# Kernel optimization log

Measured on AMD Instinct MI355X. Metric: run time of the kernel, lower is better.

## Reference

```python
import jax, jax.numpy as jnp
import numpy as np

B, L, H, S, D = 2, 4096, 16, 64, 128  # batch, seq, num_heads, num_states, head_dim


def setup_inputs() -> dict:
    key = jax.random.key(0)
    k1, k2, k3 = jax.random.split(key, 3)
    return {
        "x": jax.random.normal(k1, (B, L, H, D), dtype=jnp.float32),
        "weight": jax.random.normal(k2, (H, S, D), dtype=jnp.float32),   # nn.Parameter torch.randn
        "bias": jax.random.normal(k3, (H, S), dtype=jnp.float32),
    }


def reference(x, weight, bias):
    b, l, h, d = x.shape
    s = weight.shape[1]
    T = b * l
    # per-head linear router in fp32 (matches x.float()/weight.float() in torch)
    logits = jnp.einsum('blhd,hsd->blhs', x.astype(jnp.float32), weight.astype(jnp.float32)) \
             + bias.astype(jnp.float32)
    score = jax.nn.softmax(logits, axis=-1)                # [B,L,H,S]
    indices = jnp.argmax(score, axis=-1).astype(jnp.int32)  # [B,L,H]
    # GradTop1 forward: all-ones; straight-through backward scatters grad at argmax.
    top = jnp.take_along_axis(score, indices[..., None], axis=-1)[..., 0]
    sg_indices = top - jax.lax.stop_gradient(top) + 1.0      # forward == 1, grad -> one-hot scatter
    # histogram per head over num_states (Triton bincount equivalent)
    flat = indices.reshape(T, h)                             # [T,H]
    counts = jax.vmap(lambda v: jnp.bincount(v, length=s))(flat.T)  # [H,S]
    mean_indices = counts.astype(jnp.float32) / T
    balance_loss = s * jnp.sum(jnp.mean(mean_indices[None, None] * score, axis=(0, 1)))
    return sg_indices.astype(x.dtype), indices, balance_loss.astype(x.dtype)
```

## Files before the change

kernel.cpp:

```cpp
#include <hip/hip_runtime.h>


#define TOKENS  8192
#define NHEAD   16
#define NSTATE  64
#define DDIM    128
#define TH      (TOKENS * NHEAD)

#define WFRAG_BYTES (1u << 19)
#define REP_OFF     WFRAG_BYTES
#define REP_BYTES   65536
#define IDX_OFF     (WFRAG_BYTES + REP_BYTES)

typedef _Float16 half8 __attribute__((ext_vector_type(8)));
typedef float    f32x4 __attribute__((ext_vector_type(4)));

#define GLOAD_LDS16(gsrc, ldst)                                           \
    __builtin_amdgcn_global_load_lds(                                     \
        (const __attribute__((address_space(1))) void*)(gsrc),            \
        (__attribute__((address_space(3))) void*)(ldst), 16, 0, 0)

__device__ __forceinline__ unsigned int ordf(float f) {
    unsigned int u = __float_as_uint(f);
    return (u & 0x80000000u) ? ~u : (u | 0x80000000u);
}

__device__ __forceinline__ void split8(const f32x4 v0, const f32x4 v1,
                                       half8& hh, half8& ll) {
    #pragma unroll
    for (int j = 0; j < 4; ++j) {
        _Float16 h0 = (_Float16)v0[j];
        hh[j]     = h0;  ll[j]     = (_Float16)(v0[j] - (float)h0);
        _Float16 h1 = (_Float16)v1[j];
        hh[4 + j] = h1;  ll[4 + j] = (_Float16)(v1[j] - (float)h1);
    }
}

__global__ __launch_bounds__(256)
void prep_w(const float* __restrict__ w, half8* __restrict__ wfrag,
            float* __restrict__ rep )
{
    const int t    = blockIdx.x * 256 + threadIdx.x;
    rep[t] = 0.0f;
    const int lane = t & 63;
    const int n    = (t >> 6) & 3;
    const int ks   = (t >> 8) & 3;
    const int h    = t >> 10;
    const int s    = n * 16 + (lane & 15);
    const int k0   = ks * 32 + (lane >> 4) * 8;
    const float* src = w + (size_t)(h * NSTATE + s) * DDIM + k0;
    f32x4 v0 = *reinterpret_cast<const f32x4*>(src);
    f32x4 v1 = *reinterpret_cast<const f32x4*>(src + 4);
    half8 hv, lv;
    split8(v0, v1, hv, lv);
    const size_t hb = (size_t)h * 2048;
    const int fb = (ks * 4 + n) * 2;
    wfrag[hb + (size_t)fb * 64 + lane]       = hv;
    wfrag[hb + (size_t)(fb + 1) * 64 + lane] = lv;
}

__global__ __launch_bounds__(256)
void router_mfma(const float* __restrict__ x,
                 const half8* __restrict__ wfrag,
                 const float* __restrict__ bias,
                 float* __restrict__ idx_scr,
                 float* __restrict__ repf,
                 float* __restrict__ repc)
{
    __shared__ __align__(16) unsigned char smem[32768];

    const int blk  = blockIdx.x;
    const int h    = blk & 15;
    const int grp  = blk >> 4;
    const int tid  = threadIdx.x;
    const int wave = __builtin_amdgcn_readfirstlane(tid >> 6);
    const int lane = tid & 63;
    const int col  = lane & 15;
    const int kg   = lane >> 4;
    const int base = grp * 128;

    {
        const char* wsrc = (const char*)wfrag + (size_t)h * 32768;
        #pragma unroll
        for (int i = 0; i < 8; ++i) {
            const int off = (wave * 8 + i) * 1024;
            GLOAD_LDS16(wsrc + off + lane * 16, smem + off);
        }
    }

    const float b0 = bias[h * NSTATE +  0 + col];
    const float b1 = bias[h * NSTATE + 16 + col];
    const float b2 = bias[h * NSTATE + 32 + col];
    const float b3 = bias[h * NSTATE + 48 + col];

    __syncthreads();

    const size_t srow = (size_t)(NHEAD * DDIM);
    float sc[4] = {0.f, 0.f, 0.f, 0.f};
    int   cn[4] = {0, 0, 0, 0};

    #pragma unroll
    for (int tt = 0; tt < 2; ++tt) {
        const int tokb = base + (wave + 4 * tt) * 16;

        const float* arow = x + (size_t)(tokb + col) * srow + h * DDIM + kg * 8;
        f32x4 g[4][2];
        #pragma unroll
        for (int ks = 0; ks < 4; ++ks) {
            g[ks][0] = *reinterpret_cast<const f32x4*>(arow + ks * 32);
            g[ks][1] = *reinterpret_cast<const f32x4*>(arow + ks * 32 + 4);
        }

        f32x4 acc[4];
        #pragma unroll
        for (int n = 0; n < 4; ++n) {
            f32x4 z = {0.f, 0.f, 0.f, 0.f};
            acc[n] = z;
        }

        #pragma unroll
        for (int ks = 0; ks < 4; ++ks) {
            half8 ah, al;
            split8(g[ks][0], g[ks][1], ah, al);
            #pragma unroll
            for (int n = 0; n < 4; ++n) {
                const int fo = (ks * 4 + n) * 2048 + lane * 16;
                half8 bh = *reinterpret_cast<const half8*>(smem + fo);
                half8 bl = *reinterpret_cast<const half8*>(smem + fo + 1024);
                acc[n] = __builtin_amdgcn_mfma_f32_16x16x32_f16(ah, bh, acc[n], 0, 0, 0);
                acc[n] = __builtin_amdgcn_mfma_f32_16x16x32_f16(ah, bl, acc[n], 0, 0, 0);
                acc[n] = __builtin_amdgcn_mfma_f32_16x16x32_f16(al, bh, acc[n], 0, 0, 0);
            }
        }

        int my_idx = 0;
        #pragma unroll
        for (int rg = 0; rg < 4; ++rg) {
            float L0 = acc[0][rg] + b0;
            float L1 = acc[1][rg] + b1;
            float L2 = acc[2][rg] + b2;
            float L3 = acc[3][rg] + b3;

            unsigned long long k0 = ((unsigned long long)ordf(L0) << 6) | (unsigned)(63 - ( 0 + col));
            unsigned long long k1 = ((unsigned long long)ordf(L1) << 6) | (unsigned)(63 - (16 + col));
            unsigned long long k2 = ((unsigned long long)ordf(L2) << 6) | (unsigned)(63 - (32 + col));
            unsigned long long k3 = ((unsigned long long)ordf(L3) << 6) | (unsigned)(63 - (48 + col));
            unsigned long long ka = k0 > k1 ? k0 : k1;
            unsigned long long kb = k2 > k3 ? k2 : k3;
            unsigned long long kk = ka > kb ? ka : kb;
            #pragma unroll
            for (int d = 1; d <= 8; d <<= 1) {
                unsigned long long o = __shfl_xor(kk, d);
                kk = kk > o ? kk : o;
            }
            const int idx = 63 - (int)(kk & 63ull);

            float e0 = __expf(L0), e1 = __expf(L1), e2 = __expf(L2), e3 = __expf(L3);
            float sm = (e0 + e1) + (e2 + e3);
            #pragma unroll
            for (int d = 1; d <= 8; d <<= 1) sm += __shfl_xor(sm, d);
            const float rinv = __builtin_amdgcn_rcpf(sm);
            sc[0] += e0 * rinv; sc[1] += e1 * rinv;
            sc[2] += e2 * rinv; sc[3] += e3 * rinv;

            cn[0] += (idx ==  0 + col);
            cn[1] += (idx == 16 + col);
            cn[2] += (idx == 32 + col);
            cn[3] += (idx == 48 + col);

            if (col == rg) my_idx = idx;
        }
        if (col < 4)
            idx_scr[(size_t)h * TOKENS + tokb + (kg << 2) + col] = (float)my_idx;
    }

    #pragma unroll
    for (int n = 0; n < 4; ++n) {
        sc[n] += __shfl_xor(sc[n], 16);
        sc[n] += __shfl_xor(sc[n], 32);
        cn[n] += __shfl_xor(cn[n], 16);
        cn[n] += __shfl_xor(cn[n], 32);
    }
    if (kg == 0) {
        const int rep = ((blk << 2) | wave) & 7;
        #pragma unroll
        for (int n = 0; n < 4; ++n) {
            atomicAdd(repf + rep * 1024 + h * 64 + n * 16 + col, sc[n]);
            atomicAdd(repc + rep * 1024 + h * 64 + n * 16 + col, (float)cn[n]);
        }
    }
}

__global__ __launch_bounds__(256)
void finale(const float* __restrict__ idx_scr,
            const float* __restrict__ repf,
            const float* __restrict__ repc,
            float* __restrict__ out)
{
    const int b   = blockIdx.x;
    const int tid = threadIdx.x;

    if (b < 32) {
        __shared__ float tl[256 * 17];
        #pragma unroll
        for (int hh = 0; hh < 16; ++hh)
            tl[tid * 17 + hh] = idx_scr[(size_t)hh * TOKENS + b * 256 + tid];
        __syncthreads();
        #pragma unroll
        for (int k = 0; k < 16; ++k) {
            const int i = k * 256 + tid;
            out[(size_t)TH + (size_t)b * 4096 + i] = tl[(i >> 4) * 17 + (i & 15)];
            out[(size_t)b * 4096 + i] = 1.0f;
        }
    } else {
        float part = 0.0f;
        for (int j = tid; j < NHEAD * NSTATE; j += 256) {
            float cf = 0.f, cc = 0.f;
            #pragma unroll
            for (int r = 0; r < 8; ++r) {
                cf += repf[r * 1024 + j];
                cc += repc[r * 1024 + j];
            }
            part += cf * cc;
        }
        #pragma unroll
        for (int d = 1; d <= 32; d <<= 1)
            part += __shfl_xor(part, d);
        __shared__ float red[4];
        const int wv = tid >> 6, lane = tid & 63;
        if (lane == 0) red[wv] = part;
        __syncthreads();
        if (tid == 0) {
            const float tot = red[0] + red[1] + red[2] + red[3];
            const float T = (float)TOKENS;
            out[2 * (size_t)TH] = tot * ((float)NSTATE / (T * T));
        }
    }
}

extern "C" void kernel_launch(void* const* d_in, const int* in_sizes, int n_in,
                              void* d_out, int out_size, void* d_ws, size_t ws_size,
                              hipStream_t stream)
{
    const float* x    = (const float*)d_in[0];
    const float* w    = (const float*)d_in[1];
    const float* bias = (const float*)d_in[2];
    float* out = (float*)d_out;

    half8* wfrag   = (half8*)d_ws;
    float* rep     = (float*)((char*)d_ws + REP_OFF);
    float* repf    = rep;
    float* repc    = rep + 8192;
    float* idx_scr = (float*)((char*)d_ws + IDX_OFF);

    prep_w<<<dim3(64), dim3(256), 0, stream>>>(w, wfrag, rep);
    router_mfma<<<dim3(1024), dim3(256), 0, stream>>>(x, wfrag, bias,
                                                      idx_scr, repf, repc);
    finale<<<dim3(33), dim3(256), 0, stream>>>(idx_scr, repf, repc, out);
}
```

Measured before the change: 30.43 us.

## Switch router to 32x32 MFMA with weights as A operand and in-register softmax

Replaces the 16x16x32 MFMA tiling with 32x32x16 MFMA, where the weight fragments form the A operand and the tokens form B. Each lane then holds one token's logits, so the argmax and softmax sum need only a single cross-half shuffle instead of 16-lane butterflies. Bias is pre-laid out in the accumulator fragment order by prep_w and used as the initial accumulator. Score column sums use DPP reductions, and the histogram uses LDS atomics followed by one per-block global atomic pass. This changes fragment layouts throughout, so index mapping errors are possible.

Result: faster. 29.39 us (-3.4%).

```diff
diff --git a/kernel.cpp b/kernel.cpp
--- a/kernel.cpp
+++ b/kernel.cpp
@@ -8,22 +8,20 @@
 #define TH      (TOKENS * NHEAD)
 
 #define WFRAG_BYTES (1u << 19)
-#define REP_OFF     WFRAG_BYTES
+#define BFRAG_OFF   WFRAG_BYTES
+#define BFRAG_BYTES 4096
+#define REP_OFF     (WFRAG_BYTES + BFRAG_BYTES)
 #define REP_BYTES   65536
-#define IDX_OFF     (WFRAG_BYTES + REP_BYTES)
-
-typedef _Float16 half8 __attribute__((ext_vector_type(8)));
-typedef float    f32x4 __attribute__((ext_vector_type(4)));
+#define IDX_OFF     (REP_OFF + REP_BYTES)
+
+typedef _Float16 half8  __attribute__((ext_vector_type(8)));
+typedef float    f32x4  __attribute__((ext_vector_type(4)));
+typedef float    f32x16 __attribute__((ext_vector_type(16)));
 
 #define GLOAD_LDS16(gsrc, ldst)                                           \
     __builtin_amdgcn_global_load_lds(                                     \
         (const __attribute__((address_space(1))) void*)(gsrc),            \
         (__attribute__((address_space(3))) void*)(ldst), 16, 0, 0)
-
-__device__ __forceinline__ unsigned int ordf(float f) {
-    unsigned int u = __float_as_uint(f);
-    return (u & 0x80000000u) ? ~u : (u | 0x80000000u);
-}
 
 __device__ __forceinline__ void split8(const f32x4 v0, const f32x4 v1,
                                        half8& hh, half8& ll) {
@@ -36,38 +34,57 @@
     }
 }
 
+__device__ __forceinline__ float dpp_sum32(float v) {
+    float t;
+    t = __int_as_float(__builtin_amdgcn_update_dpp(0, __float_as_int(v), 0x111, 0xf, 0xf, true)); v += t;
+    t = __int_as_float(__builtin_amdgcn_update_dpp(0, __float_as_int(v), 0x112, 0xf, 0xf, true)); v += t;
+    t = __int_as_float(__builtin_amdgcn_update_dpp(0, __float_as_int(v), 0x114, 0xf, 0xf, true)); v += t;
+    t = __int_as_float(__builtin_amdgcn_update_dpp(0, __float_as_int(v), 0x118, 0xf, 0xf, true)); v += t;
+    t = __int_as_float(__builtin_amdgcn_update_dpp(0, __float_as_int(v), 0x142, 0xf, 0xf, true)); v += t;
+    return v;
+}
+
 __global__ __launch_bounds__(256)
-void prep_w(const float* __restrict__ w, half8* __restrict__ wfrag,
-            float* __restrict__ rep )
-{
-    const int t    = blockIdx.x * 256 + threadIdx.x;
+void prep_w(const float* __restrict__ w, const float* __restrict__ bias,
+            half8* __restrict__ wfrag, float* __restrict__ bfrag,
+            float* __restrict__ rep)
+{
+    const int t = blockIdx.x * 256 + threadIdx.x;
     rep[t] = 0.0f;
-    const int lane = t & 63;
-    const int n    = (t >> 6) & 3;
-    const int ks   = (t >> 8) & 3;
-    const int h    = t >> 10;
-    const int s    = n * 16 + (lane & 15);
-    const int k0   = ks * 32 + (lane >> 4) * 8;
+    const int lane  = t & 63;
+    const int half_ = (t >> 6) & 1;
+    const int ks    = (t >> 7) & 7;
+    const int h     = t >> 10;
+    const int s     = half_ * 32 + (lane & 31);
+    const int k0    = ks * 16 + (lane >> 5) * 8;
     const float* src = w + (size_t)(h * NSTATE + s) * DDIM + k0;
     f32x4 v0 = *reinterpret_cast<const f32x4*>(src);
     f32x4 v1 = *reinterpret_cast<const f32x4*>(src + 4);
     half8 hv, lv;
     split8(v0, v1, hv, lv);
-    const size_t hb = (size_t)h * 2048;
-    const int fb = (ks * 4 + n) * 2;
-    wfrag[hb + (size_t)fb * 64 + lane]       = hv;
-    wfrag[hb + (size_t)(fb + 1) * 64 + lane] = lv;
+    const size_t fb = (size_t)h * 2048 + (size_t)((ks * 4 + half_ * 2)) * 64;
+    wfrag[fb + lane]      = hv;
+    wfrag[fb + 64 + lane] = lv;
+
+    if (t < 1024) {
+        const int h2 = t >> 6, hi2 = (t >> 5) & 1, j = t & 31;
+        const int tau = j >> 4, r = j & 15;
+        const int s2 = (r & 3) + ((r >> 2) << 3) + (hi2 << 2) + (tau << 5);
+        bfrag[t] = bias[h2 * NSTATE + s2];
+    }
 }
 
 __global__ __launch_bounds__(256)
 void router_mfma(const float* __restrict__ x,
                  const half8* __restrict__ wfrag,
-                 const float* __restrict__ bias,
+                 const float* __restrict__ bfrag,
                  float* __restrict__ idx_scr,
                  float* __restrict__ repf,
                  float* __restrict__ repc)
 {
     __shared__ __align__(16) unsigned char smem[32768];
+    __shared__ unsigned int hist[64];
+    __shared__ __align__(16) float ssums[4][64];
 
     const int blk  = blockIdx.x;
     const int h    = blk & 15;
@@ -75,119 +92,106 @@
     const int tid  = threadIdx.x;
     const int wave = __builtin_amdgcn_readfirstlane(tid >> 6);
     const int lane = tid & 63;
-    const int col  = lane & 15;
-    const int kg   = lane >> 4;
-    const int base = grp * 128;
+    const int tk   = lane & 31;
+    const int hi   = lane >> 5;
+    const int tokb = grp * 128 + wave * 32;
 
     {
         const char* wsrc = (const char*)wfrag + (size_t)h * 32768;
         #pragma unroll
         for (int i = 0; i < 8; ++i) {
-            const int off = (wave * 8 + i) * 1024;
-            GLOAD_LDS16(wsrc + off + lane * 16, smem + off);
-        }
-    }
-
-    const float b0 = bias[h * NSTATE +  0 + col];
-    const float b1 = bias[h * NSTATE + 16 + col];
-    const float b2 = bias[h * NSTATE + 32 + col];
-    const float b3 = bias[h * NSTATE + 48 + col];
+            const int off = (i * 256 + tid) * 16;
+            GLOAD_LDS16(wsrc + off, smem + off);
+        }
+    }
+    if (tid < 64) hist[tid] = 0;
+
+    const float* bf = bfrag + ((h << 1) | hi) * 32;
+    f32x16 acc0, acc1;
+    #pragma unroll
+    for (int r = 0; r < 16; ++r) { acc0[r] = bf[r]; acc1[r] = bf[16 + r]; }
+
+    const float* xrow = x + (size_t)(tokb + tk) * (NHEAD * DDIM) + h * DDIM + hi * 8;
 
     __syncthreads();
 
-    const size_t srow = (size_t)(NHEAD * DDIM);
-    float sc[4] = {0.f, 0.f, 0.f, 0.f};
-    int   cn[4] = {0, 0, 0, 0};
-
-    #pragma unroll
-    for (int tt = 0; tt < 2; ++tt) {
-        const int tokb = base + (wave + 4 * tt) * 16;
-
-        const float* arow = x + (size_t)(tokb + col) * srow + h * DDIM + kg * 8;
-        f32x4 g[4][2];
-        #pragma unroll
-        for (int ks = 0; ks < 4; ++ks) {
-            g[ks][0] = *reinterpret_cast<const f32x4*>(arow + ks * 32);
-            g[ks][1] = *reinterpret_cast<const f32x4*>(arow + ks * 32 + 4);
-        }
-
-        f32x4 acc[4];
-        #pragma unroll
-        for (int n = 0; n < 4; ++n) {
-            f32x4 z = {0.f, 0.f, 0.f, 0.f};
-            acc[n] = z;
-        }
-
-        #pragma unroll
-        for (int ks = 0; ks < 4; ++ks) {
-            half8 ah, al;
-            split8(g[ks][0], g[ks][1], ah, al);
+    #pragma unroll
+    for (int ks = 0; ks < 8; ++ks) {
+        half8 wh0 = *reinterpret_cast<const half8*>(smem + (ks * 4 + 0) * 1024 + lane * 16);
+        half8 wl0 = *reinterpret_cast<const half8*>(smem + (ks * 4 + 1) * 1024 + lane * 16);
+        half8 wh1 = *reinterpret_cast<const half8*>(smem + (ks * 4 + 2) * 1024 + lane * 16);
+        half8 wl1 = *reinterpret_cast<const half8*>(smem + (ks * 4 + 3) * 1024 + lane * 16);
+        f32x4 g0 = *reinterpret_cast<const f32x4*>(xrow + ks * 16);
+        f32x4 g1 = *reinterpret_cast<const f32x4*>(xrow + ks * 16 + 4);
+        half8 xh, xl;
+        split8(g0, g1, xh, xl);
+        acc0 = __builtin_amdgcn_mfma_f32_32x32x16_f16(wh0, xh, acc0, 0, 0, 0);
+        acc0 = __builtin_amdgcn_mfma_f32_32x32x16_f16(wh0, xl, acc0, 0, 0, 0);
+        acc0 = __builtin_amdgcn_mfma_f32_32x32x16_f16(wl0, xh, acc0, 0, 0, 0);
+        acc1 = __builtin_amdgcn_mfma_f32_32x32x16_f16(wh1, xh, acc1, 0, 0, 0);
+        acc1 = __builtin_amdgcn_mfma_f32_32x32x16_f16(wh1, xl, acc1, 0, 0, 0);
+        acc1 = __builtin_amdgcn_mfma_f32_32x32x16_f16(wl1, xh, acc1, 0, 0, 0);
+    }
+
+    float mx = acc1[15];
+    #pragma unroll
+    for (int r = 14; r >= 0; --r) mx = fmaxf(mx, acc1[r]);
+    #pragma unroll
+    for (int r = 15; r >= 0; --r) mx = fmaxf(mx, acc0[r]);
+
+    int idx = 0;
+    #pragma unroll
+    for (int r = 15; r >= 0; --r) {
+        const int s = 32 + (r & 3) + ((r >> 2) << 3) + (hi << 2);
+        idx = (acc1[r] == mx) ? s : idx;
+    }
+    #pragma unroll
+    for (int r = 15; r >= 0; --r) {
+        const int s = (r & 3) + ((r >> 2) << 3) + (hi << 2);
+        idx = (acc0[r] == mx) ? s : idx;
+    }
+    {
+        const float omx  = __shfl_xor(mx, 32);
+        const int   oidx = __shfl_xor(idx, 32);
+        if (omx > mx || (omx == mx && oidx < idx)) { mx = omx; idx = oidx; }
+    }
+
+    float sm = 0.f;
+    #pragma unroll
+    for (int r = 0; r < 16; ++r) { acc0[r] = __expf(acc0[r]); sm += acc0[r]; }
+    #pragma unroll
+    for (int r = 0; r < 16; ++r) { acc1[r] = __expf(acc1[r]); sm += acc1[r]; }
+    sm += __shfl_xor(sm, 32);
+    const float rinv = __builtin_amdgcn_rcpf(sm);
+
+    #pragma unroll
+    for (int r = 0; r < 16; ++r) {
+        acc0[r] = dpp_sum32(acc0[r] * rinv);
+        acc1[r] = dpp_sum32(acc1[r] * rinv);
+    }
+    if ((lane & 31) == 31) {
+        #pragma unroll
+        for (int g = 0; g < 4; ++g) {
+            f32x4 p0, p1;
             #pragma unroll
-            for (int n = 0; n < 4; ++n) {
-                const int fo = (ks * 4 + n) * 2048 + lane * 16;
-                half8 bh = *reinterpret_cast<const half8*>(smem + fo);
-                half8 bl = *reinterpret_cast<const half8*>(smem + fo + 1024);
-                acc[n] = __builtin_amdgcn_mfma_f32_16x16x32_f16(ah, bh, acc[n], 0, 0, 0);
-                acc[n] = __builtin_amdgcn_mfma_f32_16x16x32_f16(ah, bl, acc[n], 0, 0, 0);
-                acc[n] = __builtin_amdgcn_mfma_f32_16x16x32_f16(al, bh, acc[n], 0, 0, 0);
-            }
-        }
-
-        int my_idx = 0;
-        #pragma unroll
-        for (int rg = 0; rg < 4; ++rg) {
-            float L0 = acc[0][rg] + b0;
-            float L1 = acc[1][rg] + b1;
-            float L2 = acc[2][rg] + b2;
-            float L3 = acc[3][rg] + b3;
-
-            unsigned long long k0 = ((unsigned long long)ordf(L0) << 6) | (unsigned)(63 - ( 0 + col));
-            unsigned long long k1 = ((unsigned long long)ordf(L1) << 6) | (unsigned)(63 - (16 + col));
-            unsigned long long k2 = ((unsigned long long)ordf(L2) << 6) | (unsigned)(63 - (32 + col));
-            unsigned long long k3 = ((unsigned long long)ordf(L3) << 6) | (unsigned)(63 - (48 + col));
-            unsigned long long ka = k0 > k1 ? k0 : k1;
-            unsigned long long kb = k2 > k3 ? k2 : k3;
-            unsigned long long kk = ka > kb ? ka : kb;
-            #pragma unroll
-            for (int d = 1; d <= 8; d <<= 1) {
-                unsigned long long o = __shfl_xor(kk, d);
-                kk = kk > o ? kk : o;
-            }
-            const int idx = 63 - (int)(kk & 63ull);
-
-            float e0 = __expf(L0), e1 = __expf(L1), e2 = __expf(L2), e3 = __expf(L3);
-            float sm = (e0 + e1) + (e2 + e3);
-            #pragma unroll
-            for (int d = 1; d <= 8; d <<= 1) sm += __shfl_xor(sm, d);
-            const float rinv = __builtin_amdgcn_rcpf(sm);
-            sc[0] += e0 * rinv; sc[1] += e1 * rinv;
-            sc[2] += e2 * rinv; sc[3] += e3 * rinv;
-
-            cn[0] += (idx ==  0 + col);
-            cn[1] += (idx == 16 + col);
-            cn[2] += (idx == 32 + col);
-            cn[3] += (idx == 48 + col);
-
-            if (col == rg) my_idx = idx;
-        }
-        if (col < 4)
-            idx_scr[(size_t)h * TOKENS + tokb + (kg << 2) + col] = (float)my_idx;
-    }
-
-    #pragma unroll
-    for (int n = 0; n < 4; ++n) {
-        sc[n] += __shfl_xor(sc[n], 16);
-        sc[n] += __shfl_xor(sc[n], 32);
-        cn[n] += __shfl_xor(cn[n], 16);
-        cn[n] += __shfl_xor(cn[n], 32);
-    }
-    if (kg == 0) {
-        const int rep = ((blk << 2) | wave) & 7;
-        #pragma unroll
-        for (int n = 0; n < 4; ++n) {
-            atomicAdd(repf + rep * 1024 + h * 64 + n * 16 + col, sc[n]);
-            atomicAdd(repc + rep * 1024 + h * 64 + n * 16 + col, (float)cn[n]);
-        }
+            for (int i = 0; i < 4; ++i) { p0[i] = acc0[g * 4 + i]; p1[i] = acc1[g * 4 + i]; }
+            *reinterpret_cast<f32x4*>(&ssums[wave][(g << 3) + (hi << 2)])      = p0;
+            *reinterpret_cast<f32x4*>(&ssums[wave][32 + (g << 3) + (hi << 2)]) = p1;
+        }
+    }
+
+    if (hi == 0) {
+        atomicAdd(&hist[idx], 1u);
+        idx_scr[(size_t)h * TOKENS + tokb + tk] = (float)idx;
+    }
+
+    __syncthreads();
+    if (wave == 0) {
+        const float sv = ssums[0][lane] + ssums[1][lane] + ssums[2][lane] + ssums[3][lane];
+        const float cv = (float)hist[lane];
+        const int rep = blk & 7;
+        atomicAdd(repf + rep * 1024 + h * 64 + lane, sv);
+        atomicAdd(repc + rep * 1024 + h * 64 + lane, cv);
     }
 }
 
@@ -248,13 +252,14 @@
     float* out = (float*)d_out;
 
     half8* wfrag   = (half8*)d_ws;
+    float* bfrag   = (float*)((char*)d_ws + BFRAG_OFF);
     float* rep     = (float*)((char*)d_ws + REP_OFF);
     float* repf    = rep;
     float* repc    = rep + 8192;
     float* idx_scr = (float*)((char*)d_ws + IDX_OFF);
 
-    prep_w<<<dim3(64), dim3(256), 0, stream>>>(w, wfrag, rep);
-    router_mfma<<<dim3(1024), dim3(256), 0, stream>>>(x, wfrag, bias,
+    prep_w<<<dim3(64), dim3(256), 0, stream>>>(w, bias, wfrag, bfrag, rep);
+    router_mfma<<<dim3(1024), dim3(256), 0, stream>>>(x, wfrag, bfrag,
                                                       idx_scr, repf, repc);
     finale<<<dim3(33), dim3(256), 0, stream>>>(idx_scr, repf, repc, out);
 }
```
